# Performance work log

Measured on AMD Instinct MI355X. Metric: run time of the kernel, lower is better.

Reference implementation:

```python
import jax, jax.numpy as jnp
import numpy as np

B, S, D, H = 2, 2048, 1024, 16
DK = D // H  # 64


def setup_inputs() -> dict:
    key = jax.random.key(0)
    ks = jax.random.split(key, 5)
    query_input = jax.random.normal(ks[0], (B, S, D), dtype=jnp.float32)
    # additive mask: 1.0 where attention is disallowed (causal upper triangle)
    mask = jnp.triu(jnp.ones((S, S), dtype=jnp.float32), k=1)[None, None, :, :]
    scale = 1.0 / np.sqrt(D)
    wq = jax.random.normal(ks[1], (D, D), dtype=jnp.float32) * scale
    wk = jax.random.normal(ks[2], (D, D), dtype=jnp.float32) * scale
    wv = jax.random.normal(ks[3], (D, D), dtype=jnp.float32) * scale
    wo = jax.random.normal(ks[4], (D, D), dtype=jnp.float32) * scale
    return {"query_input": query_input, "mask": mask, "wq": wq, "wk": wk, "wv": wv, "wo": wo}


def _split_heads(x):
    # [B, S, D] -> [B, H, S, DK]
    b, s, _ = x.shape
    return x.reshape(b, s, H, DK).transpose(0, 2, 1, 3)


def reference(query_input, mask, wq, wk, wv, wo):
    # self-attention: key_input = value_input = query_input
    q = _split_heads(query_input @ wq)  # [B, H, S, DK]
    k = _split_heads(query_input @ wk)
    v = _split_heads(query_input @ wv)
    scores = jnp.einsum('bhqd,bhkd->bhqk', q, k) / jnp.sqrt(jnp.float32(DK))
    scores = scores + mask * (-1e9)
    attn = jax.nn.softmax(scores, axis=-1)
    out = jnp.einsum('bhqk,bhkd->bhqd', attn, v)  # [B, H, S, DK]
    out = out.transpose(0, 2, 1, 3).reshape(query_input.shape[0], -1, D)
    return out @ wo
```

## Files before the change

kernel.cpp:

```cpp
#include <hip/hip_runtime.h>

typedef __attribute__((ext_vector_type(8))) short bf16x8;
typedef __attribute__((ext_vector_type(4))) float f32x4;
typedef __attribute__((ext_vector_type(4))) unsigned short u16x4;

#define S_LEN 2048
#define D_DIM 1024
#define NHEAD 16
#define DK 64
#define BH 32
#define MROWS 4096

__device__ __forceinline__ unsigned short f2bf(float f) {
    unsigned int u = __float_as_uint(f);
    u += 0x7fffu + ((u >> 16) & 1u);
    return (unsigned short)(u >> 16);
}

__device__ __forceinline__ unsigned int pk_bf16(float a, float b) {
    unsigned int r;
    asm("v_cvt_pk_bf16_f32 %0, %1, %2" : "=v"(r) : "v"(a), "v"(b));
    return r;
}

__device__ __forceinline__ void gload16(const void* g, void* l) {
    __builtin_amdgcn_global_load_lds(
        (const __attribute__((address_space(1))) void*)g,
        (__attribute__((address_space(3))) void*)l, 16, 0, 0);
}

__global__ __launch_bounds__(256) void cast_x_kernel(const float* __restrict__ X,
                                                     unsigned short* __restrict__ Xb) {
    int idx = blockIdx.x * 256 + threadIdx.x;
    float4 v = ((const float4*)X)[idx];
    u16x4 o;
    o.x = f2bf(v.x); o.y = f2bf(v.y); o.z = f2bf(v.z); o.w = f2bf(v.w);
    ((u16x4*)Xb)[idx] = o;
}

__global__ __launch_bounds__(256) void wtrans_kernel(const float* __restrict__ wq,
                                                     const float* __restrict__ wk,
                                                     const float* __restrict__ wv,
                                                     const float* __restrict__ wo,
                                                     unsigned short* __restrict__ Wt) {
    int z = blockIdx.z;
    const float* W = (z == 0) ? wq : (z == 1) ? wk : (z == 2) ? wv : wo;
    unsigned short* O = Wt + (size_t)z * D_DIM * D_DIM;
    __shared__ float t[32][33];
    int tx = threadIdx.x, ty = threadIdx.y;
    int bx = blockIdx.x * 32;
    int by = blockIdx.y * 32;
#pragma unroll
    for (int i = 0; i < 4; ++i)
        t[ty + i * 8][tx] = W[(size_t)(by + ty + i * 8) * D_DIM + bx + tx];
    __syncthreads();
#pragma unroll
    for (int i = 0; i < 4; ++i)
        O[(size_t)(bx + ty + i * 8) * D_DIM + by + tx] = f2bf(t[tx][ty + i * 8]);
}

__device__ __forceinline__ void gemm_mainloop(const unsigned short* __restrict__ A,
                                              const unsigned short* __restrict__ Bt,
                                              int K, int m0, int n0,
                                              unsigned short* As, unsigned short* Bs,
                                              f32x4 acc[4][4]) {
    const int tid = threadIdx.x;
    const int lane = tid & 63, wid = tid >> 6;
    const int wr = wid >> 1, wc = wid & 1;
    const int fr = lane & 15, fk = (lane >> 4) * 8;
    for (int k0 = 0; k0 < K; k0 += 32) {
        __syncthreads();
#pragma unroll
        for (int c = 0; c < 2; ++c) {
            int idx = c * 256 + tid;
            int row = idx >> 2;
            int col = (idx & 3) * 8;
            int base = (c * 256 + wid * 64) * 8;
            gload16(&A[(size_t)(m0 + row) * K + k0 + col], &As[base]);
            gload16(&Bt[(size_t)(n0 + row) * K + k0 + col], &Bs[base]);
        }
        __syncthreads();
        bf16x8 af[4], bfr[4];
#pragma unroll
        for (int i = 0; i < 4; ++i)
            af[i] = *(const bf16x8*)&As[(wr * 64 + i * 16 + fr) * 32 + fk];
#pragma unroll
        for (int j = 0; j < 4; ++j)
            bfr[j] = *(const bf16x8*)&Bs[(wc * 64 + j * 16 + fr) * 32 + fk];
#pragma unroll
        for (int i = 0; i < 4; ++i)
#pragma unroll
            for (int j = 0; j < 4; ++j)
                acc[i][j] = __builtin_amdgcn_mfma_f32_16x16x32_bf16(af[i], bfr[j], acc[i][j], 0, 0, 0);
    }
}

#define QSCALE 0.18033688011112042f
__global__ __launch_bounds__(256) void gemm_qkv_kernel(const unsigned short* __restrict__ Xb,
                                                       const unsigned short* __restrict__ Wt,
                                                       unsigned short* __restrict__ QKV) {
    __shared__ __align__(16) unsigned short As[128 * 32];
    __shared__ __align__(16) unsigned short Bs[128 * 32];
    const unsigned short* Bt = Wt + (size_t)blockIdx.z * D_DIM * D_DIM;
    unsigned short* Out = QKV + (size_t)blockIdx.z * MROWS * D_DIM;
    int m0 = blockIdx.y * 128, n0 = blockIdx.x * 128;
    f32x4 acc[4][4] = {};
    gemm_mainloop(Xb, Bt, D_DIM, m0, n0, As, Bs, acc);
    const float qs = (blockIdx.z == 0) ? QSCALE : 1.0f;
    const int lane = threadIdx.x & 63, wid = threadIdx.x >> 6;
    const int wr = wid >> 1, wc = wid & 1;
#pragma unroll
    for (int i = 0; i < 4; ++i)
#pragma unroll
        for (int j = 0; j < 4; ++j)
#pragma unroll
            for (int r = 0; r < 4; ++r) {
                int gm = m0 + wr * 64 + i * 16 + (lane >> 4) * 4 + r;
                int gn = n0 + wc * 64 + j * 16 + (lane & 15);
                Out[(size_t)gm * D_DIM + gn] = f2bf(acc[i][j][r] * qs);
            }
}

__global__ __launch_bounds__(256) void vtrans_kernel(const unsigned short* __restrict__ V,
                                                     unsigned short* __restrict__ Vt) {
    __shared__ unsigned short tile[64][65];
    int bh = blockIdx.y;
    int b = bh >> 4, h = bh & 15;
    int s0 = blockIdx.x * 64;
    int t = threadIdx.x;
#pragma unroll
    for (int i = 0; i < 16; ++i) {
        int idx = i * 256 + t;
        int row = idx >> 6, col = idx & 63;
        tile[row][col] = V[((size_t)(b * S_LEN) + s0 + row) * D_DIM + h * DK + col];
    }
    __syncthreads();
#pragma unroll
    for (int i = 0; i < 16; ++i) {
        int idx = i * 256 + t;
        int dr = idx >> 6, sc = idx & 63;
        Vt[((size_t)bh * DK + dr) * S_LEN + s0 + sc] = tile[sc][dr];
    }
}

__global__ __launch_bounds__(512, 4) void attn_kernel(const unsigned short* __restrict__ QKV,
                                                      const unsigned short* __restrict__ Vt,
                                                      unsigned short* __restrict__ AO) {
    const int bh = blockIdx.x;
    const int qi = 15 - (int)blockIdx.y;
    const int tid = threadIdx.x, lane = tid & 63, wid = tid >> 6;
    const int fr = lane & 15, fkg = lane >> 4, fk = fkg * 8;
    const unsigned short* Q = QKV;
    const unsigned short* Kd = QKV + (size_t)MROWS * D_DIM;

    __shared__ __align__(16) unsigned short Ks[2][64][64];
    __shared__ __align__(16) unsigned short Vs[2][64][64];
    __shared__ __align__(16) unsigned short Ps[8][16][64];

    const int b = bh >> 4, h = bh & 15;
    const int rsw  = fr & 7;
    const int off0 = (fkg ^ rsw) * 8;
    const int off1 = ((4 + fkg) ^ rsw) * 8;

    const int srow = tid >> 3;
    const int scol = ((tid & 7) ^ (srow & 7)) * 8;
    const int sbase = wid * 512;

    const int q0 = qi * 128;
    const int qr = q0 + wid * 16;

    bf16x8 qf0 = *(const bf16x8*)&Q[((size_t)(b * S_LEN) + qr + fr) * D_DIM + h * DK + fk];
    bf16x8 qf1 = *(const bf16x8*)&Q[((size_t)(b * S_LEN) + qr + fr) * D_DIM + h * DK + 32 + fk];

    f32x4 o[4] = {};
    float m = -1e30f, l = 0.f;
    const int ntiles = 2 * qi + 2;
    int buf = 0;

    gload16(&Kd[((size_t)(b * S_LEN) + srow) * D_DIM + h * DK + scol], &Ks[0][0][0] + sbase);
    gload16(&Vt[((size_t)bh * DK + srow) * S_LEN + scol], &Vs[0][0][0] + sbase);
    __syncthreads();

    for (int t = 0; t < ntiles; ++t) {
        if (t + 1 < ntiles) {
            const int ktn = (t + 1) * 64;
            gload16(&Kd[((size_t)(b * S_LEN) + ktn + srow) * D_DIM + h * DK + scol],
                    &Ks[buf ^ 1][0][0] + sbase);
            gload16(&Vt[((size_t)bh * DK + srow) * S_LEN + ktn + scol],
                    &Vs[buf ^ 1][0][0] + sbase);
        }

        f32x4 s4[4];
        __builtin_amdgcn_s_setprio(1);
#pragma unroll
        for (int nj = 0; nj < 4; ++nj) {
            const unsigned short* krow = &Ks[buf][nj * 16 + fr][0];
            bf16x8 kf0 = *(const bf16x8*)&krow[off0];
            bf16x8 kf1 = *(const bf16x8*)&krow[off1];
            f32x4 z = {};
            z = __builtin_amdgcn_mfma_f32_16x16x32_bf16(kf0, qf0, z, 0, 0, 0);
            z = __builtin_amdgcn_mfma_f32_16x16x32_bf16(kf1, qf1, z, 0, 0, 0);
            s4[nj] = z;
        }
        __builtin_amdgcn_s_setprio(0);

        if (64 * t + 63 > qr) {
            const int qoff = qr + fr - 64 * t;
#pragma unroll
            for (int nj = 0; nj < 4; ++nj)
#pragma unroll
                for (int r = 0; r < 4; ++r)
                    s4[nj][r] = (nj * 16 + fkg * 4 + r > qoff) ? -1e30f : s4[nj][r];
        }

        float m0_ = fmaxf(fmaxf(s4[0][0], s4[0][1]), fmaxf(s4[0][2], s4[0][3]));
        float m1_ = fmaxf(fmaxf(s4[1][0], s4[1][1]), fmaxf(s4[1][2], s4[1][3]));
        float m2_ = fmaxf(fmaxf(s4[2][0], s4[2][1]), fmaxf(s4[2][2], s4[2][3]));
        float m3_ = fmaxf(fmaxf(s4[3][0], s4[3][1]), fmaxf(s4[3][2], s4[3][3]));
        float mt = fmaxf(fmaxf(m0_, m1_), fmaxf(m2_, m3_));
        mt = fmaxf(mt, __shfl_xor(mt, 16, 64));
        mt = fmaxf(mt, __shfl_xor(mt, 32, 64));
        if (!__all(mt <= m + 8.0f)) {
            float mn = fmaxf(m, mt);
            float corr = exp2f(m - mn);
            m = mn;
            l *= corr;
            o[0] *= corr; o[1] *= corr; o[2] *= corr; o[3] *= corr;
        }
        float ps = 0.f;
        unsigned int pw[4][2];
#pragma unroll
        for (int nj = 0; nj < 4; ++nj) {
            float p0 = exp2f(s4[nj][0] - m);
            float p1 = exp2f(s4[nj][1] - m);
            float p2 = exp2f(s4[nj][2] - m);
            float p3 = exp2f(s4[nj][3] - m);
            ps += (p0 + p1) + (p2 + p3);
            pw[nj][0] = pk_bf16(p0, p1);
            pw[nj][1] = pk_bf16(p2, p3);
        }
        ps += __shfl_xor(ps, 16, 64);
        ps += __shfl_xor(ps, 32, 64);
        l += ps;

#pragma unroll
        for (int nj = 0; nj < 4; ++nj) {
            int chunk = nj * 2 + (fkg >> 1);
            int el = (fkg & 1) * 4;
            *(uint2*)&Ps[wid][fr][((chunk ^ rsw) << 3) + el] = make_uint2(pw[nj][0], pw[nj][1]);
        }
        bf16x8 pf0 = *(const bf16x8*)&Ps[wid][fr][off0];
        bf16x8 pf1 = *(const bf16x8*)&Ps[wid][fr][off1];
        __builtin_amdgcn_s_setprio(1);
#pragma unroll
        for (int j = 0; j < 4; ++j) {
            const unsigned short* vrow = &Vs[buf][j * 16 + fr][0];
            bf16x8 vf0 = *(const bf16x8*)&vrow[off0];
            bf16x8 vf1 = *(const bf16x8*)&vrow[off1];
            o[j] = __builtin_amdgcn_mfma_f32_16x16x32_bf16(vf0, pf0, o[j], 0, 0, 0);
            o[j] = __builtin_amdgcn_mfma_f32_16x16x32_bf16(vf1, pf1, o[j], 0, 0, 0);
        }
        __builtin_amdgcn_s_setprio(0);

        __syncthreads();
        buf ^= 1;
    }

    float inv = 1.0f / l;
    size_t rowoff = ((size_t)(b * S_LEN) + qr + fr) * D_DIM + h * DK;
#pragma unroll
    for (int j = 0; j < 4; ++j) {
        u16x4 w;
        w.x = f2bf(o[j][0] * inv); w.y = f2bf(o[j][1] * inv);
        w.z = f2bf(o[j][2] * inv); w.w = f2bf(o[j][3] * inv);
        *(u16x4*)&AO[rowoff + j * 16 + fkg * 4] = w;
    }
}

__global__ __launch_bounds__(256) void gemm_out_kernel(const unsigned short* __restrict__ AO,
                                                       const unsigned short* __restrict__ Wot,
                                                       float* __restrict__ out) {
    __shared__ __align__(16) unsigned short As[128 * 32];
    __shared__ __align__(16) unsigned short Bs[128 * 32];
    int m0 = blockIdx.y * 128, n0 = blockIdx.x * 128;
    f32x4 acc[4][4] = {};
    gemm_mainloop(AO, Wot, D_DIM, m0, n0, As, Bs, acc);
    const int lane = threadIdx.x & 63, wid = threadIdx.x >> 6;
    const int wr = wid >> 1, wc = wid & 1;
#pragma unroll
    for (int i = 0; i < 4; ++i)
#pragma unroll
        for (int j = 0; j < 4; ++j)
#pragma unroll
            for (int r = 0; r < 4; ++r) {
                int gm = m0 + wr * 64 + i * 16 + (lane >> 4) * 4 + r;
                int gn = n0 + wc * 64 + j * 16 + (lane & 15);
                out[(size_t)gm * D_DIM + gn] = acc[i][j][r];
            }
}

extern "C" void kernel_launch(void* const* d_in, const int* in_sizes, int n_in,
                              void* d_out, int out_size, void* d_ws, size_t ws_size,
                              hipStream_t stream) {
    (void)in_sizes; (void)n_in; (void)out_size; (void)ws_size;
    const float* X  = (const float*)d_in[0];
    const float* wq = (const float*)d_in[2];
    const float* wk = (const float*)d_in[3];
    const float* wv = (const float*)d_in[4];
    const float* wo = (const float*)d_in[5];

    char* ws = (char*)d_ws;
    unsigned short* Xb  = (unsigned short*)(ws);
    unsigned short* Wt  = (unsigned short*)(ws + ((size_t)8  << 20));
    unsigned short* QKV = (unsigned short*)(ws + ((size_t)16 << 20));
    unsigned short* Vt  = (unsigned short*)(ws + ((size_t)40 << 20));
    unsigned short* AO  = (unsigned short*)(ws + ((size_t)48 << 20));
    float* out = (float*)d_out;

    cast_x_kernel<<<4096, 256, 0, stream>>>(X, Xb);
    wtrans_kernel<<<dim3(32, 32, 4), dim3(32, 8), 0, stream>>>(wq, wk, wv, wo, Wt);
    gemm_qkv_kernel<<<dim3(8, 32, 3), 256, 0, stream>>>(Xb, Wt, QKV);
    vtrans_kernel<<<dim3(32, 32), 256, 0, stream>>>(QKV + (size_t)2 * MROWS * D_DIM, Vt);
    attn_kernel<<<dim3(32, 16), 512, 0, stream>>>(QKV, Vt, AO);
    gemm_out_kernel<<<dim3(8, 32), 256, 0, stream>>>(AO, Wt + (size_t)3 * D_DIM * D_DIM, out);
}
```

Before: 122.3 us.

## Widen GEMM K-tile with swizzled LDS and double attention KV tile to 128

The GEMM mainloop now stages 64-wide K slices with an XOR-swizzled shared-memory layout, which halves the barrier count and is meant to reduce bank conflicts. The attention kernel processes 128-key tiles per iteration instead of 64, so it loops and synchronises half as often and only masks the final diagonal tile. It also reorders query-block scheduling so heavy and light causal blocks are interleaved. The costs are more shared memory per block, which may lower occupancy, and more register pressure.

```diff
diff --git a/kernel.cpp b/kernel.cpp
--- a/kernel.cpp
+++ b/kernel.cpp
@@ -67,31 +67,35 @@
     const int tid = threadIdx.x;
     const int lane = tid & 63, wid = tid >> 6;
     const int wr = wid >> 1, wc = wid & 1;
-    const int fr = lane & 15, fk = (lane >> 4) * 8;
-    for (int k0 = 0; k0 < K; k0 += 32) {
+    const int fr = lane & 15, fkg = lane >> 4;
+    const int rsw = fr & 7;
+    for (int k0 = 0; k0 < K; k0 += 64) {
         __syncthreads();
 #pragma unroll
-        for (int c = 0; c < 2; ++c) {
-            int idx = c * 256 + tid;
-            int row = idx >> 2;
-            int col = (idx & 3) * 8;
+        for (int c = 0; c < 4; ++c) {
+            int i = c * 256 + tid;
+            int row = i >> 3;
+            int col = ((i & 7) ^ (row & 7)) * 8;
             int base = (c * 256 + wid * 64) * 8;
             gload16(&A[(size_t)(m0 + row) * K + k0 + col], &As[base]);
             gload16(&Bt[(size_t)(n0 + row) * K + k0 + col], &Bs[base]);
         }
         __syncthreads();
-        bf16x8 af[4], bfr[4];
-#pragma unroll
-        for (int i = 0; i < 4; ++i)
-            af[i] = *(const bf16x8*)&As[(wr * 64 + i * 16 + fr) * 32 + fk];
-#pragma unroll
-        for (int j = 0; j < 4; ++j)
-            bfr[j] = *(const bf16x8*)&Bs[(wc * 64 + j * 16 + fr) * 32 + fk];
-#pragma unroll
-        for (int i = 0; i < 4; ++i)
+#pragma unroll
+        for (int kk = 0; kk < 2; ++kk) {
+            bf16x8 af[4], bfr[4];
+#pragma unroll
+            for (int i = 0; i < 4; ++i)
+                af[i] = *(const bf16x8*)&As[(wr * 64 + i * 16 + fr) * 64 + (((kk * 4 + fkg) ^ rsw) * 8)];
 #pragma unroll
             for (int j = 0; j < 4; ++j)
-                acc[i][j] = __builtin_amdgcn_mfma_f32_16x16x32_bf16(af[i], bfr[j], acc[i][j], 0, 0, 0);
+                bfr[j] = *(const bf16x8*)&Bs[(wc * 64 + j * 16 + fr) * 64 + (((kk * 4 + fkg) ^ rsw) * 8)];
+#pragma unroll
+            for (int i = 0; i < 4; ++i)
+#pragma unroll
+                for (int j = 0; j < 4; ++j)
+                    acc[i][j] = __builtin_amdgcn_mfma_f32_16x16x32_bf16(af[i], bfr[j], acc[i][j], 0, 0, 0);
+        }
     }
 }
 
@@ -99,8 +103,8 @@
 __global__ __launch_bounds__(256) void gemm_qkv_kernel(const unsigned short* __restrict__ Xb,
                                                        const unsigned short* __restrict__ Wt,
                                                        unsigned short* __restrict__ QKV) {
-    __shared__ __align__(16) unsigned short As[128 * 32];
-    __shared__ __align__(16) unsigned short Bs[128 * 32];
+    __shared__ __align__(16) unsigned short As[128 * 64];
+    __shared__ __align__(16) unsigned short Bs[128 * 64];
     const unsigned short* Bt = Wt + (size_t)blockIdx.z * D_DIM * D_DIM;
     unsigned short* Out = QKV + (size_t)blockIdx.z * MROWS * D_DIM;
     int m0 = blockIdx.y * 128, n0 = blockIdx.x * 128;
@@ -147,14 +151,15 @@
                                                       const unsigned short* __restrict__ Vt,
                                                       unsigned short* __restrict__ AO) {
     const int bh = blockIdx.x;
-    const int qi = 15 - (int)blockIdx.y;
+    const int y = blockIdx.y;
+    const int qi = (y < 8) ? (15 - y) : (y - 8);
     const int tid = threadIdx.x, lane = tid & 63, wid = tid >> 6;
     const int fr = lane & 15, fkg = lane >> 4, fk = fkg * 8;
     const unsigned short* Q = QKV;
     const unsigned short* Kd = QKV + (size_t)MROWS * D_DIM;
 
-    __shared__ __align__(16) unsigned short Ks[2][64][64];
-    __shared__ __align__(16) unsigned short Vs[2][64][64];
+    __shared__ __align__(16) unsigned short Ks[2][128][64];
+    __shared__ __align__(16) unsigned short Vs[2][64][128];
     __shared__ __align__(16) unsigned short Ps[8][16][64];
 
     const int b = bh >> 4, h = bh & 15;
@@ -162,9 +167,13 @@
     const int off0 = (fkg ^ rsw) * 8;
     const int off1 = ((4 + fkg) ^ rsw) * 8;
 
-    const int srow = tid >> 3;
-    const int scol = ((tid & 7) ^ (srow & 7)) * 8;
-    const int sbase = wid * 512;
+    const int i0 = tid, i1 = 512 + tid;
+    const int kr0 = i0 >> 3, kc0 = ((i0 & 7) ^ (kr0 & 7)) * 8;
+    const int kr1 = i1 >> 3, kc1 = ((i1 & 7) ^ (kr1 & 7)) * 8;
+    const int vr0 = i0 >> 4, vc0 = ((i0 & 15) ^ (vr0 & 15)) * 8;
+    const int vr1 = i1 >> 4, vc1 = ((i1 & 15) ^ (vr1 & 15)) * 8;
+    const int sb0 = (wid * 64) * 8;
+    const int sb1 = (512 + wid * 64) * 8;
 
     const int q0 = qi * 128;
     const int qr = q0 + wid * 16;
@@ -174,26 +183,31 @@
 
     f32x4 o[4] = {};
     float m = -1e30f, l = 0.f;
-    const int ntiles = 2 * qi + 2;
-    int buf = 0;
-
-    gload16(&Kd[((size_t)(b * S_LEN) + srow) * D_DIM + h * DK + scol], &Ks[0][0][0] + sbase);
-    gload16(&Vt[((size_t)bh * DK + srow) * S_LEN + scol], &Vs[0][0][0] + sbase);
+    const int ntiles = qi + 1;
+
+    const unsigned short* kb = Kd + (size_t)(b * S_LEN) * D_DIM + h * DK;
+    const unsigned short* vb = Vt + (size_t)bh * DK * S_LEN;
+
+    gload16(kb + (size_t)kr0 * D_DIM + kc0, &Ks[0][0][0] + sb0);
+    gload16(kb + (size_t)kr1 * D_DIM + kc1, &Ks[0][0][0] + sb1);
+    gload16(vb + (size_t)vr0 * S_LEN + vc0, &Vs[0][0][0] + sb0);
+    gload16(vb + (size_t)vr1 * S_LEN + vc1, &Vs[0][0][0] + sb1);
     __syncthreads();
 
     for (int t = 0; t < ntiles; ++t) {
+        const int buf = t & 1;
         if (t + 1 < ntiles) {
-            const int ktn = (t + 1) * 64;
-            gload16(&Kd[((size_t)(b * S_LEN) + ktn + srow) * D_DIM + h * DK + scol],
-                    &Ks[buf ^ 1][0][0] + sbase);
-            gload16(&Vt[((size_t)bh * DK + srow) * S_LEN + ktn + scol],
-                    &Vs[buf ^ 1][0][0] + sbase);
-        }
-
-        f32x4 s4[4];
+            const int kt = (t + 1) * 128;
+            gload16(kb + (size_t)(kt + kr0) * D_DIM + kc0, &Ks[buf ^ 1][0][0] + sb0);
+            gload16(kb + (size_t)(kt + kr1) * D_DIM + kc1, &Ks[buf ^ 1][0][0] + sb1);
+            gload16(vb + (size_t)vr0 * S_LEN + kt + vc0, &Vs[buf ^ 1][0][0] + sb0);
+            gload16(vb + (size_t)vr1 * S_LEN + kt + vc1, &Vs[buf ^ 1][0][0] + sb1);
+        }
+
+        f32x4 s4[8];
         __builtin_amdgcn_s_setprio(1);
 #pragma unroll
-        for (int nj = 0; nj < 4; ++nj) {
+        for (int nj = 0; nj < 8; ++nj) {
             const unsigned short* krow = &Ks[buf][nj * 16 + fr][0];
             bf16x8 kf0 = *(const bf16x8*)&krow[off0];
             bf16x8 kf1 = *(const bf16x8*)&krow[off1];
@@ -204,20 +218,21 @@
         }
         __builtin_amdgcn_s_setprio(0);
 
-        if (64 * t + 63 > qr) {
-            const int qoff = qr + fr - 64 * t;
-#pragma unroll
-            for (int nj = 0; nj < 4; ++nj)
+        if (t == ntiles - 1) {
+            const int qoff = wid * 16 + fr;
+#pragma unroll
+            for (int nj = 0; nj < 8; ++nj)
 #pragma unroll
                 for (int r = 0; r < 4; ++r)
                     s4[nj][r] = (nj * 16 + fkg * 4 + r > qoff) ? -1e30f : s4[nj][r];
         }
 
-        float m0_ = fmaxf(fmaxf(s4[0][0], s4[0][1]), fmaxf(s4[0][2], s4[0][3]));
-        float m1_ = fmaxf(fmaxf(s4[1][0], s4[1][1]), fmaxf(s4[1][2], s4[1][3]));
-        float m2_ = fmaxf(fmaxf(s4[2][0], s4[2][1]), fmaxf(s4[2][2], s4[2][3]));
-        float m3_ = fmaxf(fmaxf(s4[3][0], s4[3][1]), fmaxf(s4[3][2], s4[3][3]));
-        float mt = fmaxf(fmaxf(m0_, m1_), fmaxf(m2_, m3_));
+        float mg[8];
+#pragma unroll
+        for (int nj = 0; nj < 8; ++nj)
+            mg[nj] = fmaxf(fmaxf(s4[nj][0], s4[nj][1]), fmaxf(s4[nj][2], s4[nj][3]));
+        float mt = fmaxf(fmaxf(fmaxf(mg[0], mg[1]), fmaxf(mg[2], mg[3])),
+                         fmaxf(fmaxf(mg[4], mg[5]), fmaxf(mg[6], mg[7])));
         mt = fmaxf(mt, __shfl_xor(mt, 16, 64));
         mt = fmaxf(mt, __shfl_xor(mt, 32, 64));
         if (!__all(mt <= m + 8.0f)) {
@@ -228,9 +243,9 @@
             o[0] *= corr; o[1] *= corr; o[2] *= corr; o[3] *= corr;
         }
         float ps = 0.f;
-        unsigned int pw[4][2];
-#pragma unroll
-        for (int nj = 0; nj < 4; ++nj) {
+        unsigned int pw[8][2];
+#pragma unroll
+        for (int nj = 0; nj < 8; ++nj) {
             float p0 = exp2f(s4[nj][0] - m);
             float p1 = exp2f(s4[nj][1] - m);
             float p2 = exp2f(s4[nj][2] - m);
@@ -244,26 +259,29 @@
         l += ps;
 
 #pragma unroll
-        for (int nj = 0; nj < 4; ++nj) {
-            int chunk = nj * 2 + (fkg >> 1);
-            int el = (fkg & 1) * 4;
-            *(uint2*)&Ps[wid][fr][((chunk ^ rsw) << 3) + el] = make_uint2(pw[nj][0], pw[nj][1]);
-        }
-        bf16x8 pf0 = *(const bf16x8*)&Ps[wid][fr][off0];
-        bf16x8 pf1 = *(const bf16x8*)&Ps[wid][fr][off1];
-        __builtin_amdgcn_s_setprio(1);
-#pragma unroll
-        for (int j = 0; j < 4; ++j) {
-            const unsigned short* vrow = &Vs[buf][j * 16 + fr][0];
-            bf16x8 vf0 = *(const bf16x8*)&vrow[off0];
-            bf16x8 vf1 = *(const bf16x8*)&vrow[off1];
-            o[j] = __builtin_amdgcn_mfma_f32_16x16x32_bf16(vf0, pf0, o[j], 0, 0, 0);
-            o[j] = __builtin_amdgcn_mfma_f32_16x16x32_bf16(vf1, pf1, o[j], 0, 0, 0);
-        }
-        __builtin_amdgcn_s_setprio(0);
+        for (int hf = 0; hf < 2; ++hf) {
+#pragma unroll
+            for (int nj = 0; nj < 4; ++nj) {
+                int chunk = nj * 2 + (fkg >> 1);
+                int el = (fkg & 1) * 4;
+                *(uint2*)&Ps[wid][fr][((chunk ^ rsw) << 3) + el] =
+                    make_uint2(pw[hf * 4 + nj][0], pw[hf * 4 + nj][1]);
+            }
+            bf16x8 pf0 = *(const bf16x8*)&Ps[wid][fr][off0];
+            bf16x8 pf1 = *(const bf16x8*)&Ps[wid][fr][off1];
+            __builtin_amdgcn_s_setprio(1);
+#pragma unroll
+            for (int j = 0; j < 4; ++j) {
+                const unsigned short* vrow = &Vs[buf][j * 16 + fr][0];
+                bf16x8 vf0 = *(const bf16x8*)&vrow[((hf * 8 + fkg) ^ fr) * 8];
+                bf16x8 vf1 = *(const bf16x8*)&vrow[((hf * 8 + 4 + fkg) ^ fr) * 8];
+                o[j] = __builtin_amdgcn_mfma_f32_16x16x32_bf16(vf0, pf0, o[j], 0, 0, 0);
+                o[j] = __builtin_amdgcn_mfma_f32_16x16x32_bf16(vf1, pf1, o[j], 0, 0, 0);
+            }
+            __builtin_amdgcn_s_setprio(0);
+        }
 
         __syncthreads();
-        buf ^= 1;
     }
 
     float inv = 1.0f / l;
@@ -280,8 +298,8 @@
 __global__ __launch_bounds__(256) void gemm_out_kernel(const unsigned short* __restrict__ AO,
                                                        const unsigned short* __restrict__ Wot,
                                                        float* __restrict__ out) {
-    __shared__ __align__(16) unsigned short As[128 * 32];
-    __shared__ __align__(16) unsigned short Bs[128 * 32];
+    __shared__ __align__(16) unsigned short As[128 * 64];
+    __shared__ __align__(16) unsigned short Bs[128 * 64];
     int m0 = blockIdx.y * 128, n0 = blockIdx.x * 128;
     f32x4 acc[4][4] = {};
     gemm_mainloop(AO, Wot, D_DIM, m0, n0, As, Bs, acc);
```

After: 131.2 us. +7.3%, slower.
